# Performance work log

Measured on AMD Instinct MI355X. Metric: run time of the kernel, lower is better.

Reference implementation:

```python
import jax, jax.numpy as jnp
import numpy as np
from jax import lax

B, CIN, H, W = 64, 3, 64, 64
HID = 128          # hidden_dim == embedding_dim
K = 1024           # num_embeddings
BETA = 0.25        # commitment cost


def _conv(x, w, b, stride):
    # torch Conv2d, padding=0, NCHW / OIHW weights
    y = lax.conv_general_dilated(x, w, (stride, stride), 'VALID',
                                 dimension_numbers=('NCHW', 'OIHW', 'NCHW'))
    return y + b[None, :, None, None]


def _conv_transpose(x, w, b, stride):
    # torch ConvTranspose2d, padding=0; w is [Cin, Cout, kh, kw] (torch layout)
    kh, kw = w.shape[2], w.shape[3]
    w2 = jnp.flip(w, (2, 3)).transpose(1, 0, 2, 3)  # -> OIHW, spatially flipped
    y = lax.conv_general_dilated(x, w2, (1, 1),
                                 [(kh - 1, kh - 1), (kw - 1, kw - 1)],
                                 lhs_dilation=(stride, stride),
                                 dimension_numbers=('NCHW', 'OIHW', 'NCHW'))
    return y + b[None, :, None, None]


def setup_inputs() -> dict:
    key = jax.random.key(0)
    ks = jax.random.split(key, 10)
    s = 0.05
    return {
        'x':      jax.random.normal(ks[0], (B, CIN, H, W), jnp.float32),
        'enc_w1': jax.random.normal(ks[1], (HID, CIN, 4, 4), jnp.float32) * s,
        'enc_b1': jnp.zeros((HID,), jnp.float32),
        'enc_w2': jax.random.normal(ks[2], (HID, HID, 2, 2), jnp.float32) * s,
        'enc_b2': jnp.zeros((HID,), jnp.float32),
        'codebook': jax.random.uniform(ks[3], (K, HID), jnp.float32,
                                       minval=-1.0 / K, maxval=1.0 / K),
        'dec_w1': jax.random.normal(ks[4], (HID, HID, 2, 2), jnp.float32) * s,
        'dec_b1': jnp.zeros((HID,), jnp.float32),
        'dec_w2': jax.random.normal(ks[5], (HID, CIN, 4, 4), jnp.float32) * s,
        'dec_b2': jnp.zeros((CIN,), jnp.float32),
    }


def reference(x, enc_w1, enc_b1, enc_w2, enc_b2, codebook,
              dec_w1, dec_b1, dec_w2, dec_b2):
    # ---- encoder ----
    z = jax.nn.relu(_conv(x, enc_w1, enc_b1, 2))
    z = jax.nn.relu(_conv(z, enc_w2, enc_b2, 1))   # [B, HID, 30, 30]

    # ---- vector quantizer (faithful to torch reshape semantics) ----
    D = HID
    flat = z.reshape(-1, D)                        # [N, D], C-order rows
    # squared euclidean distances (argmin identical to torch.cdist argmin)
    d2 = (jnp.sum(flat * flat, axis=1, keepdims=True)
          - 2.0 * flat @ codebook.T
          + jnp.sum(codebook * codebook, axis=1)[None, :])  # [N, K]
    idx = jnp.argmin(d2, axis=1)                   # [N]
    quantized = codebook[idx].reshape(z.shape)

    e_latent = jnp.mean((lax.stop_gradient(quantized) - z) ** 2)
    q_latent = jnp.mean((quantized - lax.stop_gradient(z)) ** 2)
    loss = q_latent + BETA * e_latent

    q_st = z + lax.stop_gradient(quantized - z)    # straight-through

    n = flat.shape[0]
    avg_probs = jnp.zeros((K,), z.dtype).at[idx].add(1.0) / n
    perplexity = jnp.exp(-jnp.sum(avg_probs * jnp.log(avg_probs + 1e-10)))

    # ---- decoder ----
    y = jax.nn.relu(_conv_transpose(q_st, dec_w1, dec_b1, 1))
    x_recon = _conv_transpose(y, dec_w2, dec_b2, 2)  # [B, 3, 64, 64]
    return x_recon, loss, perplexity
```

## Files before the change

### kernel.cpp

```cpp
#include <hip/hip_runtime.h>

#define B_    64
#define CIN_  3
#define HW_   64
#define HID_  128
#define K_    1024
#define H1_   31
#define H2_   30
#define NROWS_ 57600
#define NELEM_ 7372800

typedef __bf16 bf16_t;
typedef __attribute__((ext_vector_type(8))) __bf16 bf16x8;
typedef __attribute__((ext_vector_type(4))) float f32x4;

__global__ __launch_bounds__(256) void wprep_k(const float* __restrict__ ew1,
    const float* __restrict__ ew2, const float* __restrict__ dw1,
    const float* __restrict__ dw2, const float* __restrict__ cb,
    bf16_t* __restrict__ wc1, bf16_t* __restrict__ wc2,
    bf16_t* __restrict__ wd1, bf16_t* __restrict__ wt2,
    bf16_t* __restrict__ cbb, float* __restrict__ cnorm,
    unsigned* __restrict__ hist, float* __restrict__ sse) {
  int id = blockIdx.x * 256 + threadIdx.x;
  int t = id >> 14, co = (id >> 7) & 127, ci = id & 127;
  wc2[id] = (bf16_t)ew2[(co * 128 + ci) * 4 + t];
  wd1[id] = (bf16_t)dw1[(ci * 128 + co) * 4 + (3 - t)];
  if (id < 8192) {
    int n = id >> 9, k = id & 511;
    int tap = k >> 7, c = k & 127;
    if (n < 12) {
      int nco = n >> 2, ph = (n >> 1) & 1, pw = n & 1;
      int off = (tap >> 1) * 8 + (tap & 1) * 2;
      wt2[id] = (bf16_t)dw2[c * 48 + nco * 16 + ph * 4 + pw + off];
    } else {
      wt2[id] = (bf16_t)0.f;
    }
    int c1 = id >> 6, k1 = id & 63;
    wc1[id] = (bf16_t)(k1 < 48 ? ew1[c1 * 48 + k1] : 0.f);
  }
  if (id < K_) {
    float s0 = 0.f;
    for (int d = 0; d < HID_; d += 4) {
      float4 v = *(const float4*)&cb[id * HID_ + d];
      bf16_t tt[4] = {(bf16_t)v.x, (bf16_t)v.y, (bf16_t)v.z, (bf16_t)v.w};
      *(ushort4*)&((ushort*)cbb)[id * HID_ + d] = *(ushort4*)tt;
      float f0 = (float)tt[0], f1 = (float)tt[1];
      float f2 = (float)tt[2], f3 = (float)tt[3];
      s0 += f0 * f0 + f1 * f1 + f2 * f2 + f3 * f3;
    }
    cnorm[id] = s0;
    hist[id] = 0u;
  }
  if (id == 0) *sse = 0.f;
}

__global__ __launch_bounds__(256, 2) void conv1m_k(const float* __restrict__ x,
    const bf16_t* __restrict__ wc1, const float* __restrict__ bias,
    ushort* __restrict__ z1t) {
  __shared__ __align__(16) bf16_t as_[64 * 72];
  __shared__ __align__(16) bf16_t bs_[128 * 72];
  int b = blockIdx.x >> 4, rt = blockIdx.x & 15;
  int tid = threadIdx.x, wv = tid >> 6, ln = tid & 63;
  const float* xb = x + (size_t)b * 12288;
  #pragma unroll
  for (int it = 0; it < 16; ++it) {
    int e = it * 256 + tid;
    int p = e >> 6, k = e & 63;
    float v = 0.f;
    if (k < 48) {
      int ci = k >> 4, kh = (k >> 2) & 3, kw = k & 3;
      int row = 2 * rt + (p >> 5); if (row > 30) row = 30;
      int col = p & 31;            if (col > 30) col = 30;
      v = xb[ci * 4096 + (2 * row + kh) * 64 + 2 * col + kw];
    }
    as_[p * 72 + k] = (bf16_t)v;
  }
  {
    const float4* wg = (const float4*)wc1;
    #pragma unroll
    for (int it = 0; it < 4; ++it) {
      int fi = it * 256 + tid;
      int co = fi >> 3, k8 = fi & 7;
      *(float4*)&bs_[co * 72 + k8 * 8] = wg[fi];
    }
  }
  __syncthreads();
  int q = ln >> 4, l = ln & 15;
  f32x4 acc8[8];
  #pragma unroll
  for (int c = 0; c < 8; ++c) acc8[c] = (f32x4){0.f, 0.f, 0.f, 0.f};
  bf16x8 af[2];
  #pragma unroll
  for (int kk = 0; kk < 2; ++kk)
    af[kk] = *(const bf16x8*)&as_[(wv * 16 + l) * 72 + kk * 32 + q * 8];
  #pragma unroll
  for (int cot = 0; cot < 8; ++cot) {
    #pragma unroll
    for (int kk = 0; kk < 2; ++kk) {
      bf16x8 bf = *(const bf16x8*)&bs_[(cot * 16 + l) * 72 + kk * 32 + q * 8];
      acc8[cot] = __builtin_amdgcn_mfma_f32_16x16x32_bf16(af[kk], bf,
                                                          acc8[cot], 0, 0, 0);
    }
  }
  #pragma unroll
  for (int cot = 0; cot < 8; ++cot) {
    int co = cot * 16 + l;
    float bv = bias[co];
    #pragma unroll
    for (int r = 0; r < 4; ++r) {
      int pos = wv * 16 + q * 4 + r;
      int prow = 2 * rt + (pos >> 5), pcol = pos & 31;
      if (prow < 31 && pcol < 31) {
        float v = fmaxf(acc8[cot][r] + bv, 0.f);
        bf16_t h = (bf16_t)v;
        z1t[((size_t)(b * 1024 + prow * 32 + pcol)) * 128 + co] = *(ushort*)&h;
      }
    }
  }
}

__global__ __launch_bounds__(256, 2) void conv2m_k(const bf16_t* __restrict__ z1t,
    const bf16_t* __restrict__ wc2, const float* __restrict__ bias,
    float* __restrict__ z, ushort* __restrict__ zbuf) {
  __shared__ __align__(16) bf16_t as_[98 * 136];
  __shared__ __align__(16) bf16_t bs_[128 * 136];
  int blk = blockIdx.x;
  int b = blk / 15, rt = blk % 15;
  int tid = threadIdx.x, wv = tid >> 6, ln = tid & 63;
  const float4* src = (const float4*)(z1t + ((size_t)b * 1024 + rt * 64) * 128);
  #pragma unroll
  for (int s = 0; s < 7; ++s) {
    int f = s * 256 + tid;
    if (f < 1568) {
      int lp = f >> 4, c16 = f & 15;
      *(float4*)&as_[lp * 136 + c16 * 8] = src[f];
    }
  }
  int m = wv * 16 + (ln & 15), q = ln >> 4;
  f32x4 acc8[8];
  #pragma unroll
  for (int c = 0; c < 8; ++c) acc8[c] = (f32x4){0.f, 0.f, 0.f, 0.f};
  const float4* w4 = (const float4*)wc2;
  #pragma unroll
  for (int t = 0; t < 4; ++t) {
    __syncthreads();
    #pragma unroll
    for (int s = 0; s < 8; ++s) {
      int f = s * 256 + tid;
      int co = f >> 4, c16 = f & 15;
      *(float4*)&bs_[co * 136 + c16 * 8] = w4[t * 2048 + f];
    }
    __syncthreads();
    int off = (t >> 1) * 32 + (t & 1);
    bf16x8 af[4];
    #pragma unroll
    for (int kk = 0; kk < 4; ++kk)
      af[kk] = *(const bf16x8*)&as_[(m + off) * 136 + kk * 32 + q * 8];
    #pragma unroll
    for (int cot = 0; cot < 8; ++cot) {
      #pragma unroll
      for (int kk = 0; kk < 4; ++kk) {
        bf16x8 bf = *(const bf16x8*)&bs_[(cot * 16 + (ln & 15)) * 136 +
                                         kk * 32 + q * 8];
        acc8[cot] = __builtin_amdgcn_mfma_f32_16x16x32_bf16(af[kk], bf,
                                                            acc8[cot], 0, 0, 0);
      }
    }
  }
  #pragma unroll
  for (int cot = 0; cot < 8; ++cot) {
    int co = cot * 16 + (ln & 15);
    float bv = bias[co];
    #pragma unroll
    for (int r = 0; r < 4; ++r) {
      int mo = wv * 16 + q * 4 + r;
      int ocol = mo & 31;
      if (ocol < 30) {
        int orow = rt * 2 + (mo >> 5);
        float v = fmaxf(acc8[cot][r] + bv, 0.f);
        size_t idx = (size_t)(b * HID_ + co) * 900 + orow * 30 + ocol;
        z[idx] = v;
        bf16_t h = (bf16_t)v;
        zbuf[idx] = *(ushort*)&h;
      }
    }
  }
}

__global__ __launch_bounds__(256, 2) void vq1_k(const bf16_t* __restrict__ zb,
    const bf16_t* __restrict__ cbb, const float* __restrict__ cnorm,
    int* __restrict__ idxArr, unsigned* __restrict__ hist) {
  __shared__ __align__(16) bf16_t zs[64 * 136];
  __shared__ __align__(16) bf16_t cbs[128 * 136];
  __shared__ unsigned long long red[64 * 16];
  __shared__ float cns[K_];
  int n0 = blockIdx.x * 64;
  int tid = threadIdx.x;
  int wv = tid >> 6, ln = tid & 63;
  {
    const float4* zg4 = (const float4*)(zb + (size_t)n0 * HID_);
    #pragma unroll
    for (int s = 0; s < 4; ++s) {
      int f = s * 256 + tid;
      int row = f >> 4, seg = f & 15;
      *(float4*)&zs[row * 136 + seg * 8] = zg4[f];
    }
    ((float4*)cns)[tid] = ((const float4*)cnorm)[tid];
  }
  __syncthreads();
  bf16x8 afr[4];
  #pragma unroll
  for (int kk = 0; kk < 4; ++kk)
    afr[kk] = *(const bf16x8*)&zs[(wv * 16 + (ln & 15)) * 136 + kk * 32 +
                                  (ln >> 4) * 8];
  unsigned long long best[4] = {~0ull, ~0ull, ~0ull, ~0ull};
  const float4* cg4 = (const float4*)cbb;
  for (int c0 = 0; c0 < K_; c0 += 128) {
    __syncthreads();
    #pragma unroll
    for (int s = 0; s < 8; ++s) {
      int f = s * 256 + tid;
      int code = f >> 4, seg = f & 15;
      *(float4*)&cbs[code * 136 + seg * 8] = cg4[(c0 + code) * 16 + seg];
    }
    __syncthreads();
    #pragma unroll 2
    for (int t = 0; t < 8; ++t) {
      f32x4 acc = {0.f, 0.f, 0.f, 0.f};
      #pragma unroll
      for (int kk = 0; kk < 4; ++kk) {
        bf16x8 bfr = *(const bf16x8*)&cbs[(t * 16 + (ln & 15)) * 136 +
                                          kk * 32 + (ln >> 4) * 8];
        acc = __builtin_amdgcn_mfma_f32_16x16x32_bf16(afr[kk], bfr, acc,
                                                      0, 0, 0);
      }
      int code = c0 + t * 16 + (ln & 15);
      float cn = cns[code];
      #pragma unroll
      for (int r = 0; r < 4; ++r) {
        float dist = cn - 2.f * acc[r];
        unsigned u = __float_as_uint(dist);
        u = (u & 0x80000000u) ? ~u : (u | 0x80000000u);
        unsigned long long p = ((unsigned long long)u << 32) | (unsigned)code;
        if (p < best[r]) best[r] = p;
      }
    }
  }
  __syncthreads();
  #pragma unroll
  for (int r = 0; r < 4; ++r)
    red[(wv * 16 + (ln >> 4) * 4 + r) * 16 + (ln & 15)] = best[r];
  __syncthreads();
  if (tid < 64) {
    unsigned long long b = ~0ull;
    #pragma unroll
    for (int c = 0; c < 16; ++c) {
      unsigned long long p = red[tid * 16 + c];
      if (p < b) b = p;
    }
    int bi = (int)(b & 0xffffffffu);
    idxArr[n0 + tid] = bi;
    atomicAdd(&hist[bi], 1u);
  }
}

__global__ __launch_bounds__(256) void tqsse_k(const float4* __restrict__ z4,
    const float* __restrict__ cb, const bf16_t* __restrict__ cbb,
    const int* __restrict__ idxArr, ushort* __restrict__ qt,
    float* __restrict__ sse) {
  __shared__ ushort t[60 * 128];
  __shared__ float red4[4];
  int bid = blockIdx.x, tid = threadIdx.x;
  if (bid < 900) {
    int base = bid * 2048 + tid;
    float se = 0.f;
    #pragma unroll
    for (int it = 0; it < 8; ++it) {
      int i = base + it * 256;
      int f = i * 4;
      int n = f >> 7, d = f & 127;
      int k = idxArr[n];
      float4 zv = z4[i];
      float4 cv = *(const float4*)&cb[k * 128 + d];
      float dx = cv.x - zv.x, dy = cv.y - zv.y;
      float dz = cv.z - zv.z, dw = cv.w - zv.w;
      se += dx * dx + dy * dy + dz * dz + dw * dw;
    }
    #pragma unroll
    for (int o = 32; o > 0; o >>= 1) se += __shfl_down(se, o, 64);
    if ((tid & 63) == 0) red4[tid >> 6] = se;
    __syncthreads();
    if (tid == 0) atomicAdd(sse, red4[0] + red4[1] + red4[2] + red4[3]);
  } else if (bid < 1860) {
    int tb = bid - 900;
    int b = tb / 15, st = tb % 15;
    int s0 = st * 60;
    #pragma unroll
    for (int it = 0; it < 8; ++it) {
      int task = it * 256 + tid;
      if (task < 1920) {
        int sc = task >> 7, c = task & 127;
        int f = b * 115200 + c * 900 + s0 + sc * 4;
        int n = f >> 7, d = f & 127;
        int k = idxArr[n];
        ushort4 v = *(const ushort4*)((const ushort*)cbb + k * 128 + d);
        t[(sc * 4 + 0) * 128 + c] = v.x;
        t[(sc * 4 + 1) * 128 + c] = v.y;
        t[(sc * 4 + 2) * 128 + c] = v.z;
        t[(sc * 4 + 3) * 128 + c] = v.w;
      }
    }
    __syncthreads();
    #pragma unroll
    for (int it = 0; it < 4; ++it) {
      int task = it * 256 + tid;
      if (task < 960) {
        int sl = task >> 4, c16 = task & 15;
        int s = s0 + sl;
        int h = s / 30, w = s - h * 30;
        int p = (h + 1) * 32 + (w + 1);
        *(uint4*)&qt[((size_t)(b * 1024 + p)) * 128 + c16 * 8] =
            *(uint4*)&t[sl * 128 + c16 * 8];
      }
    }
  } else {
    int zb_ = (bid - 1860) * 4;
    uint4 zz = {0u, 0u, 0u, 0u};
    for (int e = tid; e < 4 * 124 * 16; e += 256) {
      int bb = zb_ + e / (124 * 16);
      int rem = e % (124 * 16);
      int pe = rem >> 4, s16 = rem & 15;
      int p;
      if (pe < 32) p = pe;
      else if (pe < 64) p = 31 * 32 + (pe - 32);
      else {
        int idx = pe - 64;
        p = (1 + (idx >> 1)) * 32 + ((idx & 1) ? 31 : 0);
      }
      *(uint4*)&qt[((size_t)(bb * 1024 + p)) * 128 + s16 * 8] = zz;
    }
  }
}

__global__ __launch_bounds__(256, 2) void convt1m_k(const bf16_t* __restrict__ qt,
    const bf16_t* __restrict__ wd1, const float* __restrict__ bias,
    ushort* __restrict__ yt) {
  __shared__ __align__(16) bf16_t as_[98 * 136];
  __shared__ __align__(16) bf16_t bs_[128 * 136];
  int blk = blockIdx.x;
  int b = blk >> 4, rt = blk & 15;
  int tid = threadIdx.x, wv = tid >> 6, ln = tid & 63;
  {
    uint4 zz = {0u, 0u, 0u, 0u};
    ushort* ytb = yt + (size_t)b * 1156 * 128;
    int nrows = (rt < 15) ? 2 : 1;
    int r0 = 2 * rt + 1;
    for (int e = tid; e < nrows * 48; e += 256) {
      int rr = e / 48, rem = e % 48, cc = rem / 16, s16 = rem % 16;
      int col = (cc == 0) ? 0 : (cc == 1 ? 32 : 33);
      *(uint4*)&ytb[((size_t)((r0 + rr) * 34 + col)) * 128 + s16 * 8] = zz;
    }
    if (rt == 0)
      for (int e = tid; e < 34 * 16; e += 256)
        *(uint4*)&ytb[((size_t)(e >> 4)) * 128 + (e & 15) * 8] = zz;
    if (rt == 15)
      for (int e = tid; e < 2 * 34 * 16; e += 256) {
        int rr = 32 + e / 544, rem = e % 544;
        *(uint4*)&ytb[((size_t)(rr * 34 + (rem >> 4))) * 128 + (rem & 15) * 8]
            = zz;
      }
  }
  const float4* src = (const float4*)(qt + (size_t)b * 1024 * 128);
  #pragma unroll
  for (int s = 0; s < 7; ++s) {
    int f = s * 256 + tid;
    if (f < 1568) {
      int lp = f >> 4, c16 = f & 15;
      int gr = rt * 64 + lp;
      if (gr > 1023) gr = 1023;
      *(float4*)&as_[lp * 136 + c16 * 8] = src[gr * 16 + c16];
    }
  }
  int m = wv * 16 + (ln & 15), q = ln >> 4;
  f32x4 acc8[8];
  #pragma unroll
  for (int c = 0; c < 8; ++c) acc8[c] = (f32x4){0.f, 0.f, 0.f, 0.f};
  const float4* w4 = (const float4*)wd1;
  #pragma unroll
  for (int t = 0; t < 4; ++t) {
    __syncthreads();
    #pragma unroll
    for (int s = 0; s < 8; ++s) {
      int f = s * 256 + tid;
      int co = f >> 4, c16 = f & 15;
      *(float4*)&bs_[co * 136 + c16 * 8] = w4[t * 2048 + f];
    }
    __syncthreads();
    int off = (t >> 1) * 32 + (t & 1);
    bf16x8 af[4];
    #pragma unroll
    for (int kk = 0; kk < 4; ++kk)
      af[kk] = *(const bf16x8*)&as_[(m + off) * 136 + kk * 32 + q * 8];
    #pragma unroll
    for (int cot = 0; cot < 8; ++cot) {
      #pragma unroll
      for (int kk = 0; kk < 4; ++kk) {
        bf16x8 bf = *(const bf16x8*)&bs_[(cot * 16 + (ln & 15)) * 136 +
                                         kk * 32 + q * 8];
        acc8[cot] = __builtin_amdgcn_mfma_f32_16x16x32_bf16(af[kk], bf,
                                                            acc8[cot], 0, 0, 0);
      }
    }
  }
  #pragma unroll
  for (int cot = 0; cot < 8; ++cot) {
    int co = cot * 16 + (ln & 15);
    float bv = bias[co];
    #pragma unroll
    for (int r = 0; r < 4; ++r) {
      int mo = wv * 16 + q * 4 + r;
      int orow = rt * 2 + (mo >> 5), ocol = mo & 31;
      if (orow < 31 && ocol < 31) {
        float v = fmaxf(acc8[cot][r] + bv, 0.f);
        bf16_t h = (bf16_t)v;
        yt[((size_t)b * 1156 + (orow + 1) * 34 + (ocol + 1)) * 128 + co] =
            *(ushort*)&h;
      }
    }
  }
}

__global__ __launch_bounds__(256, 2) void convt2m_k(const bf16_t* __restrict__ yt,
    const bf16_t* __restrict__ wt2, const float* __restrict__ bias,
    const unsigned* __restrict__ hist, const float* __restrict__ sse,
    float* __restrict__ out) {
  __shared__ __align__(16) bf16_t as_[128 * 136];
  __shared__ float redf[256];
  int b = blockIdx.x >> 4, rt = blockIdx.x & 15;
  int tid = threadIdx.x, wv = tid >> 6, ln = tid & 63;
  const float4* src = (const float4*)(yt + ((size_t)b * 1156 + rt * 68) * 128);
  #pragma unroll
  for (int s = 0; s < 8; ++s) {
    int f = s * 256 + tid;
    int lp = f >> 4, c16 = f & 15;
    *(float4*)&as_[lp * 136 + c16 * 8] = src[f];
  }
  __syncthreads();
  int mloc = wv * 16 + (ln & 15), q = ln >> 4;
  int qh = mloc >> 5, qw = mloc & 31;
  int base = (qh + 1) * 34 + qw + 1;
  f32x4 acc = {0.f, 0.f, 0.f, 0.f};
  #pragma unroll
  for (int kc = 0; kc < 16; ++kc) {
    int tap = kc >> 2;
    int toff = (tap & 1) + (tap >> 1) * 34;
    bf16x8 af = *(const bf16x8*)&as_[(base - toff) * 136 +
                                     (kc & 3) * 32 + q * 8];
    bf16x8 bf = *(const bf16x8*)&wt2[(size_t)(ln & 15) * 512 + kc * 32 + q * 8];
    acc = __builtin_amdgcn_mfma_f32_16x16x32_bf16(af, bf, acc, 0, 0, 0);
  }
  __syncthreads();
  float* bb = (float*)as_;
  #pragma unroll
  for (int r = 0; r < 4; ++r)
    bb[(wv * 16 + q * 4 + r) * 16 + (ln & 15)] = acc[r];
  __syncthreads();
  if (tid < 192) {
    int row_id = tid >> 4;
    int co = row_id >> 2, ohoff = row_id & 3;
    int qhl = ohoff >> 1, ph = ohoff & 1;
    float bv = bias[co];
    int ow0 = (tid & 15) * 4;
    float tmp[4];
    #pragma unroll
    for (int e = 0; e < 4; ++e) {
      int ow = ow0 + e;
      tmp[e] = bb[(qhl * 32 + (ow >> 1)) * 16 + co * 4 + ph * 2 + (ow & 1)]
               + bv;
    }
    *(float4*)&out[((size_t)(b * 3 + co)) * 4096 + (rt * 4 + ohoff) * 64 + ow0]
        = *(float4*)tmp;
  }
  if (blockIdx.x == 0) {
    float e = 0.f;
    for (int k = tid; k < K_; k += 256) {
      float p = (float)hist[k] * (1.0f / (float)NROWS_);
      e += p * logf(p + 1e-10f);
    }
    redf[tid] = e;
    __syncthreads();
    #pragma unroll
    for (int t = 128; t > 0; t >>= 1) {
      if (tid < t) redf[tid] += redf[tid + t];
      __syncthreads();
    }
    if (tid == 0) {
      out[786432] = 1.25f * (*sse) * (1.0f / (float)NELEM_);
      out[786433] = expf(-redf[0]);
    }
  }
}

extern "C" void kernel_launch(void* const* d_in, const int* in_sizes, int n_in,
                              void* d_out, int out_size, void* d_ws,
                              size_t ws_size, hipStream_t stream) {
  (void)in_sizes; (void)n_in; (void)out_size; (void)ws_size;
  const float* x   = (const float*)d_in[0];
  const float* ew1 = (const float*)d_in[1];
  const float* eb1 = (const float*)d_in[2];
  const float* ew2 = (const float*)d_in[3];
  const float* eb2 = (const float*)d_in[4];
  const float* cb  = (const float*)d_in[5];
  const float* dw1 = (const float*)d_in[6];
  const float* db1 = (const float*)d_in[7];
  const float* dw2 = (const float*)d_in[8];
  const float* db2 = (const float*)d_in[9];
  float* out = (float*)d_out;
  char* ws = (char*)d_ws;

  ushort*   yt    = (ushort*)(ws);
  float*    z     = (float*)(ws + 35684352);
  bf16_t*   z1t   = (bf16_t*)(ws + 65175552);
  bf16_t*   qt    = (bf16_t*)(ws + 65175552);
  ushort*   zbuf  = (ushort*)(ws + 81985536);
  bf16_t*   cbb   = (bf16_t*)(ws + 96731136);
  bf16_t*   wc2   = (bf16_t*)(ws + 96993280);
  bf16_t*   wd1   = (bf16_t*)(ws + 97124352);
  int*      idxArr= (int*)(ws + 97255424);
  unsigned* hist  = (unsigned*)(ws + 97485824);
  float*    cnorm = (float*)(ws + 97489920);
  float*    sse   = (float*)(ws + 97494016);
  bf16_t*   wt2   = (bf16_t*)(ws + 97497088);
  bf16_t*   wc1   = (bf16_t*)(ws + 97513472);

  wprep_k<<<dim3(256), dim3(256), 0, stream>>>(ew1, ew2, dw1, dw2, cb,
                                               wc1, wc2, wd1, wt2,
                                               cbb, cnorm, hist, sse);
  conv1m_k<<<dim3(1024), dim3(256), 0, stream>>>(x, wc1, eb1, (ushort*)z1t);
  conv2m_k<<<dim3(960), dim3(256), 0, stream>>>(z1t, wc2, eb2, z, zbuf);
  vq1_k<<<dim3(900), dim3(256), 0, stream>>>((const bf16_t*)zbuf, cbb, cnorm,
                                             idxArr, hist);
  tqsse_k<<<dim3(1876), dim3(256), 0, stream>>>((const float4*)z, cb, cbb,
                                                idxArr, (ushort*)qt, sse);
  convt1m_k<<<dim3(1024), dim3(256), 0, stream>>>(qt, wd1, db1, yt);
  convt2m_k<<<dim3(1024), dim3(256), 0, stream>>>((const bf16_t*)yt, wt2, db2,
                                                  hist, sse, out);
}
```

Measured before the change: 254.6 us.

## Compute VQ loss from argmin distance in vq kernel, drop fp32 z buffer

```diff
diff --git a/kernel.cpp b/kernel.cpp
--- a/kernel.cpp
+++ b/kernel.cpp
@@ -121,7 +121,7 @@
 
 __global__ __launch_bounds__(256, 2) void conv2m_k(const bf16_t* __restrict__ z1t,
     const bf16_t* __restrict__ wc2, const float* __restrict__ bias,
-    float* __restrict__ z, ushort* __restrict__ zbuf) {
+    ushort* __restrict__ zbuf) {
   __shared__ __align__(16) bf16_t as_[98 * 136];
   __shared__ __align__(16) bf16_t bs_[128 * 136];
   int blk = blockIdx.x;
@@ -178,10 +178,8 @@
       if (ocol < 30) {
         int orow = rt * 2 + (mo >> 5);
         float v = fmaxf(acc8[cot][r] + bv, 0.f);
-        size_t idx = (size_t)(b * HID_ + co) * 900 + orow * 30 + ocol;
-        z[idx] = v;
         bf16_t h = (bf16_t)v;
-        zbuf[idx] = *(ushort*)&h;
+        zbuf[(size_t)(b * HID_ + co) * 900 + orow * 30 + ocol] = *(ushort*)&h;
       }
     }
   }
@@ -189,7 +187,8 @@
 
 __global__ __launch_bounds__(256, 2) void vq1_k(const bf16_t* __restrict__ zb,
     const bf16_t* __restrict__ cbb, const float* __restrict__ cnorm,
-    int* __restrict__ idxArr, unsigned* __restrict__ hist) {
+    int* __restrict__ idxArr, unsigned* __restrict__ hist,
+    float* __restrict__ sse) {
   __shared__ __align__(16) bf16_t zs[64 * 136];
   __shared__ __align__(16) bf16_t cbs[128 * 136];
   __shared__ unsigned long long red[64 * 16];
@@ -261,39 +260,32 @@
     int bi = (int)(b & 0xffffffffu);
     idxArr[n0 + tid] = bi;
     atomicAdd(&hist[bi], 1u);
-  }
-}
-
-__global__ __launch_bounds__(256) void tqsse_k(const float4* __restrict__ z4,
-    const float* __restrict__ cb, const bf16_t* __restrict__ cbb,
-    const int* __restrict__ idxArr, ushort* __restrict__ qt,
-    float* __restrict__ sse) {
+    unsigned hi = (unsigned)(b >> 32);
+    unsigned orig = (hi & 0x80000000u) ? (hi & 0x7fffffffu) : ~hi;
+    float dmin = __uint_as_float(orig);
+    float zn = 0.f;
+    #pragma unroll
+    for (int s = 0; s < 16; ++s) {
+      bf16x8 v = *(const bf16x8*)&zs[tid * 136 + s * 8];
+      #pragma unroll
+      for (int e = 0; e < 8; ++e) {
+        float fv = (float)v[e];
+        zn = fmaf(fv, fv, zn);
+      }
+    }
+    float se = zn + dmin;
+    #pragma unroll
+    for (int o = 32; o > 0; o >>= 1) se += __shfl_down(se, o, 64);
+    if (tid == 0) atomicAdd(sse, se);
+  }
+}
+
+__global__ __launch_bounds__(256) void tqz_k(const bf16_t* __restrict__ cbb,
+    const int* __restrict__ idxArr, ushort* __restrict__ qt) {
   __shared__ ushort t[60 * 128];
-  __shared__ float red4[4];
   int bid = blockIdx.x, tid = threadIdx.x;
-  if (bid < 900) {
-    int base = bid * 2048 + tid;
-    float se = 0.f;
-    #pragma unroll
-    for (int it = 0; it < 8; ++it) {
-      int i = base + it * 256;
-      int f = i * 4;
-      int n = f >> 7, d = f & 127;
-      int k = idxArr[n];
-      float4 zv = z4[i];
-      float4 cv = *(const float4*)&cb[k * 128 + d];
-      float dx = cv.x - zv.x, dy = cv.y - zv.y;
-      float dz = cv.z - zv.z, dw = cv.w - zv.w;
-      se += dx * dx + dy * dy + dz * dz + dw * dw;
-    }
-    #pragma unroll
-    for (int o = 32; o > 0; o >>= 1) se += __shfl_down(se, o, 64);
-    if ((tid & 63) == 0) red4[tid >> 6] = se;
-    __syncthreads();
-    if (tid == 0) atomicAdd(sse, red4[0] + red4[1] + red4[2] + red4[3]);
-  } else if (bid < 1860) {
-    int tb = bid - 900;
-    int b = tb / 15, st = tb % 15;
+  if (bid < 960) {
+    int b = bid / 15, st = bid % 15;
     int s0 = st * 60;
     #pragma unroll
     for (int it = 0; it < 8; ++it) {
@@ -324,7 +316,7 @@
       }
     }
   } else {
-    int zb_ = (bid - 1860) * 4;
+    int zb_ = (bid - 960) * 4;
     uint4 zz = {0u, 0u, 0u, 0u};
     for (int e = tid; e < 4 * 124 * 16; e += 256) {
       int bb = zb_ + e / (124 * 16);
@@ -519,7 +511,6 @@
   char* ws = (char*)d_ws;
 
   ushort*   yt    = (ushort*)(ws);
-  float*    z     = (float*)(ws + 35684352);
   bf16_t*   z1t   = (bf16_t*)(ws + 65175552);
   bf16_t*   qt    = (bf16_t*)(ws + 65175552);
   ushort*   zbuf  = (ushort*)(ws + 81985536);
@@ -537,11 +528,10 @@
                                                wc1, wc2, wd1, wt2,
                                                cbb, cnorm, hist, sse);
   conv1m_k<<<dim3(1024), dim3(256), 0, stream>>>(x, wc1, eb1, (ushort*)z1t);
-  conv2m_k<<<dim3(960), dim3(256), 0, stream>>>(z1t, wc2, eb2, z, zbuf);
+  conv2m_k<<<dim3(960), dim3(256), 0, stream>>>(z1t, wc2, eb2, zbuf);
   vq1_k<<<dim3(900), dim3(256), 0, stream>>>((const bf16_t*)zbuf, cbb, cnorm,
-                                             idxArr, hist);
-  tqsse_k<<<dim3(1876), dim3(256), 0, stream>>>((const float4*)z, cb, cbb,
-                                                idxArr, (ushort*)qt, sse);
+                                             idxArr, hist, sse);
+  tqz_k<<<dim3(976), dim3(256), 0, stream>>>(cbb, idxArr, (ushort*)qt);
   convt1m_k<<<dim3(1024), dim3(256), 0, stream>>>(qt, wd1, db1, yt);
   convt2m_k<<<dim3(1024), dim3(256), 0, stream>>>((const bf16_t*)yt, wt2, db2,
                                                   hist, sse, out);
```

Result: faster. 231.2 us (-9.2%).
